# Kernel optimization log

Hardware: AMD Instinct MI355X
Metric: run time of the kernel (lower is better)

## Reference

```python
import jax, jax.numpy as jnp
import numpy as np

# ----- module constants (from init_kwargs) -----
PCD_RANGE = np.array([-5.0, -5.0, -2.0, 5.0, 5.0, 2.0], dtype=np.float32)
VOXEL = np.array([1.0, 1.0, 1.0], dtype=np.float32)
ANG_BINS = 8
MAX_DIS = 15
GRID = ((PCD_RANGE[3:] - PCD_RANGE[:3]) // VOXEL + 1).astype(np.int64)  # [11,11,5]
L = int(np.prod(GRID))  # 605 grid locations
LOW = PCD_RANGE[:3]


def _locs():
    ax = [np.arange(g, dtype=np.float32) for g in GRID]
    mesh = np.stack(np.meshgrid(*ax, indexing='ij'), axis=-1).reshape(-1, 3)  # [L,3]
    return jnp.asarray(LOW + mesh * VOXEL)


def _mats():
    angs = np.array([np.pi / ANG_BINS * a - np.pi / 2 for a in range(ANG_BINS)], dtype=np.float32)
    c, s = np.cos(angs), np.sin(angs)
    z, o = np.zeros_like(c), np.ones_like(c)
    m = np.stack([np.stack([c, -s, z], -1), np.stack([s, c, z], -1), np.stack([z, z, o], -1)], axis=1)
    return jnp.asarray(m)  # [A,3,3]


def setup_inputs() -> dict:
    key = jax.random.key(0)
    lo = jnp.array([-4.5, -4.5, -1.5], dtype=jnp.float32)
    hi = jnp.array([4.5, 4.5, 1.5], dtype=jnp.float32)
    pcd = jax.random.uniform(key, (8, 16384, 3), dtype=jnp.float32, minval=0.0, maxval=1.0)
    pcd = lo + pcd * (hi - lo)  # points inside the point-cloud range
    return {"pcd": pcd}


def reference(pcd):
    B, N, _ = pcd.shape
    locs = _locs()                       # [L,3]
    mats = _mats()                       # [A,3,3]
    offset = jnp.asarray(-LOW + VOXEL / 2.0)
    vox = jnp.asarray(VOXEL)

    # ---- radius count feature: count(dist <= i+1) for i in 0..MAX_DIS-1 ----
    # squared distances via gram trick -> [B,L,N] (avoids [B,L,N,3] diff tensor)
    d2 = ((pcd ** 2).sum(-1)[:, None, :] + (locs ** 2).sum(-1)[None, :, None]
          - 2.0 * jnp.einsum('bnd,ld->bln', pcd, locs))
    d = jnp.ceil(jnp.sqrt(jnp.maximum(d2, 0.0)))  # integer-valued ceil distances
    dint = jax.lax.stop_gradient(jnp.clip(d, 0, MAX_DIS + 1).astype(jnp.int32))
    hist = jax.vmap(lambda r: jnp.bincount(r, length=MAX_DIS + 2))(dint.reshape(B * L, N))
    cum = jnp.cumsum(hist.reshape(B, L, MAX_DIS + 2), axis=-1)
    feature = cum[..., 1:MAX_DIS + 1]    # [B,L,MAX_DIS], count(d <= i+1)

    # ---- rotated voxel histogram feature ----
    # pcd @ M.T for each angle: [A,B,N,3]
    rot = jnp.einsum('bnd,aed->abne', pcd, mats) + offset
    coords = jnp.floor(rot / vox)
    gz, gy = int(GRID[2]), int(GRID[1])
    flat = coords[..., 2] + coords[..., 1] * gz + coords[..., 0] * gy * gz
    idx = jax.lax.stop_gradient(flat.astype(jnp.int32))  # [A,B,N]
    # torch.histc(min=-0.5, max=L-0.5) keeps integer values in [0, L-1]
    valid = (idx >= 0) & (idx < L)
    idx_safe = jnp.where(valid, idx, L)
    A = ANG_BINS
    hr = jax.vmap(lambda r: jnp.bincount(r, length=L + 1))(idx_safe.reshape(A * B, N))
    feature_rot = hr.reshape(A, B, L + 1)[..., :L].transpose(1, 2, 0)  # [B,L,A]

    out = jnp.concatenate([feature.astype(jnp.float32),
                           feature_rot.astype(jnp.float32)], axis=-1) / N
    return out  # [B, L, MAX_DIS + ANG_BINS]
```

## Files before the change

kernel.cpp:

```cpp
#include <hip/hip_runtime.h>

#define BATCH  8
#define NPTS   16384
#define LVOX   605
#define ABINS  8
#define CH     23
#define NCOL   121
#define NBIN   14
#define BPTS   256
#define FEAT_BLOCKS (BATCH * (NPTS / BPTS))
#define ROT_CH    4
#define ROT_CHPTS (NPTS / ROT_CH)
#define ROT_BLOCKS (ABINS * BATCH * ROT_CH)

#define ROT_WS_U32  (ABINS * BATCH * LVOX)
#define FEAT_WS_U32 (BATCH * LVOX * (NBIN / 2))
#define WS_U32_TOTAL (ROT_WS_U32 + FEAT_WS_U32)

__global__ __launch_bounds__(256) void zero_kernel(unsigned* __restrict__ ws) {
    const int i = blockIdx.x * 256 + threadIdx.x;
    if (i < WS_U32_TOTAL) ws[i] = 0u;
}

__global__ __launch_bounds__(512) void main_kernel(const float* __restrict__ pcd,
                                                   int* __restrict__ rot_hist,
                                                   unsigned* __restrict__ feat_hist) {
    __shared__ unsigned hist[5][NBIN][128];
    const int bid = blockIdx.x;
    const int tid = threadIdx.x;

    if (bid < FEAT_BLOCKS) {
        const int b     = bid >> 6;
        const int outer = bid & 63;

        {
            unsigned* hp = &hist[0][0][0];
            for (int i = tid; i < 5 * NBIN * 128; i += 512) hp[i] = 0u;
        }

        const int li = tid & 127;
        const int cc = (li < NCOL) ? li : (NCOL - 1);
        const float lx = -5.0f + (float)(cc / 11);
        const float ly = -5.0f + (float)(cc % 11);
        const int pbase = __builtin_amdgcn_readfirstlane(tid >> 7) * 64;
        const float* __restrict__ pp =
            pcd + ((size_t)b * NPTS + outer * BPTS + pbase) * 3;

        __syncthreads();

#pragma unroll 4
        for (int j = 0; j < 64; ++j) {
            const float px = pp[j * 3 + 0];
            const float py = pp[j * 3 + 1];
            const float pz = pp[j * 3 + 2];
            const float dx = px - lx, dy = py - ly;
            const float rxy2 = fmaf(dy, dy, dx * dx);
            const float dz0 = pz + 2.0f;
#pragma unroll
            for (int z = 0; z < 5; ++z) {
                const float dz = dz0 - (float)z;
                const float d  = __builtin_amdgcn_sqrtf(fmaf(dz, dz, rxy2));
                const int   k  = (int)d;
                atomicAdd(&hist[z][k][li], 1u);
            }
        }
        __syncthreads();

        for (int item = tid; item < NCOL * 5 * (NBIN / 2); item += 512) {
            const int kp  = item % 7;
            const int rem = item / 7;
            const int z   = rem % 5;
            const int col = rem / 5;
            const unsigned v = hist[z][2 * kp][col] | (hist[z][2 * kp + 1][col] << 16);
            if (v) atomicAdd(&feat_hist[((size_t)b * LVOX + col * 5 + z) * 7 + kp], v);
        }
    } else {
        const int rb    = bid - FEAT_BLOCKS;
        const int ab    = rb & 63;
        const int chunk = rb >> 6;
        const int a     = ab >> 3;
        const int b     = ab & 7;

        int* h = (int*)&hist[0][0][0];
        for (int i = tid; i < LVOX; i += 512) h[i] = 0;
        __syncthreads();

        const float C[8] = { -4.3711388e-08f, 0.3826834323650898f, 0.7071067811865476f,
                             0.9238795325112867f, 1.0f, 0.9238795325112867f,
                             0.7071067811865476f, 0.3826834323650898f };
        const float S[8] = { -1.0f, -0.9238795325112867f, -0.7071067811865476f,
                             -0.3826834323650898f, 0.0f, 0.3826834323650898f,
                             0.7071067811865476f, 0.9238795325112867f };
        const float c = C[a];
        const float s = S[a];

        const float* __restrict__ p =
            pcd + ((size_t)b * NPTS + (size_t)chunk * ROT_CHPTS) * 3;

        for (int n = tid; n < ROT_CHPTS; n += 512) {
            const float x = p[n * 3 + 0];
            const float y = p[n * 3 + 1];
            const float z = p[n * 3 + 2];
            const float rx = x * c - y * s + 5.5f;
            const float ry = x * s + y * c + 5.5f;
            const float rz = z + 2.5f;
            const int icx = (int)floorf(rx);
            const int icy = (int)floorf(ry);
            const int icz = (int)floorf(rz);
            const int flat = icz + icy * 5 + icx * 55;
            if (flat >= 0 && flat < LVOX) atomicAdd(&h[flat], 1);
        }
        __syncthreads();

        int* __restrict__ dst = rot_hist + (size_t)ab * LVOX;
        for (int i = tid; i < LVOX; i += 512) {
            const int v = h[i];
            if (v) atomicAdd(&dst[i], v);
        }
    }
}

__global__ __launch_bounds__(256) void write_kernel(const int* __restrict__ rot_hist,
                                                    const unsigned* __restrict__ feat16,
                                                    float* __restrict__ out) {
    const int gt    = blockIdx.x * 256 + threadIdx.x;
    const int group = gt >> 4;
    const int q     = gt & 15;
    if (group >= BATCH * LVOX) return;
    const int b = group / LVOX;
    const int l = group % LVOX;

    int v = 0;
    if (q < NBIN) {
        const unsigned w = feat16[(size_t)group * 7 + (q >> 1)];
        v = (int)((w >> (16 * (q & 1))) & 0xFFFFu);
    }
#pragma unroll
    for (int off = 1; off < 16; off <<= 1) {
        const int t = __shfl_up(v, off, 16);
        if (q >= off) v += t;
    }
    const float inv_n = 1.0f / (float)NPTS;
    float* __restrict__ o = out + (size_t)group * CH;
    if (q < NBIN)       o[q]  = (float)v * inv_n;
    else if (q == NBIN) o[14] = 1.0f;
    if (q < 8) {
        const int r = rot_hist[((size_t)q * BATCH + b) * LVOX + l];
        o[15 + q] = (float)r * inv_n;
    }
}

extern "C" void kernel_launch(void* const* d_in, const int* in_sizes, int n_in,
                              void* d_out, int out_size, void* d_ws, size_t ws_size,
                              hipStream_t stream) {
    const float* pcd = (const float*)d_in[0];
    float* out = (float*)d_out;
    int* rot_hist = (int*)d_ws;
    unsigned* feat16 = (unsigned*)d_ws + ROT_WS_U32;

    hipLaunchKernelGGL(zero_kernel, dim3((WS_U32_TOTAL + 255) / 256), dim3(256), 0,
                       stream, (unsigned*)d_ws);
    hipLaunchKernelGGL(main_kernel, dim3(FEAT_BLOCKS + ROT_BLOCKS), dim3(512), 0,
                       stream, pcd, rot_hist, feat16);
    hipLaunchKernelGGL(write_kernel, dim3((BATCH * LVOX * 16 + 255) / 256), dim3(256),
                       0, stream, rot_hist, feat16, out);
}
```

Measured before the change: 35.61 us.

## Replace LDS atomics for two z-layers with packed register nibble counters

For z-layers 3 and 4, distance-bin counts are now kept in 64-bit registers as 4-bit nibble counters. Every 15 points these are flushed into 8-bit lanes split into even and odd bins, and then staged through shared memory instead of issuing an LDS atomic per point. This cuts LDS atomic traffic by two fifths and shrinks the histogram array. In exchange it adds 64-bit shift and add work and a more complex reduction step. Correctness relies on bin indices staying below 16 and per-thread counts not overflowing 8 bits.

```diff
diff --git a/kernel.cpp b/kernel.cpp
--- a/kernel.cpp
+++ b/kernel.cpp
@@ -17,6 +17,8 @@
 #define FEAT_WS_U32 (BATCH * LVOX * (NBIN / 2))
 #define WS_U32_TOTAL (ROT_WS_U32 + FEAT_WS_U32)
 
+#define MASK8 0x0F0F0F0F0F0F0F0Full
+
 __global__ __launch_bounds__(256) void zero_kernel(unsigned* __restrict__ ws) {
     const int i = blockIdx.x * 256 + threadIdx.x;
     if (i < WS_U32_TOTAL) ws[i] = 0u;
@@ -25,7 +27,8 @@
 __global__ __launch_bounds__(512) void main_kernel(const float* __restrict__ pcd,
                                                    int* __restrict__ rot_hist,
                                                    unsigned* __restrict__ feat_hist) {
-    __shared__ unsigned hist[5][NBIN][128];
+    __shared__ unsigned hist[3][NBIN][128];
+    __shared__ unsigned long long stag[2][2][4][129];
     const int bid = blockIdx.x;
     const int tid = threadIdx.x;
 
@@ -35,35 +38,56 @@
 
         {
             unsigned* hp = &hist[0][0][0];
-            for (int i = tid; i < 5 * NBIN * 128; i += 512) hp[i] = 0u;
+            for (int i = tid; i < 3 * NBIN * 128; i += 512) hp[i] = 0u;
         }
 
         const int li = tid & 127;
         const int cc = (li < NCOL) ? li : (NCOL - 1);
         const float lx = -5.0f + (float)(cc / 11);
         const float ly = -5.0f + (float)(cc % 11);
-        const int pbase = __builtin_amdgcn_readfirstlane(tid >> 7) * 64;
+        const int g4 = __builtin_amdgcn_readfirstlane(tid >> 7);
         const float* __restrict__ pp =
-            pcd + ((size_t)b * NPTS + outer * BPTS + pbase) * 3;
-
-        __syncthreads();
-
-#pragma unroll 4
-        for (int j = 0; j < 64; ++j) {
-            const float px = pp[j * 3 + 0];
-            const float py = pp[j * 3 + 1];
-            const float pz = pp[j * 3 + 2];
-            const float dx = px - lx, dy = py - ly;
-            const float rxy2 = fmaf(dy, dy, dx * dx);
-            const float dz0 = pz + 2.0f;
-#pragma unroll
-            for (int z = 0; z < 5; ++z) {
-                const float dz = dz0 - (float)z;
-                const float d  = __builtin_amdgcn_sqrtf(fmaf(dz, dz, rxy2));
-                const int   k  = (int)d;
-                atomicAdd(&hist[z][k][li], 1u);
-            }
-        }
+            pcd + ((size_t)b * NPTS + outer * BPTS + g4 * 64) * 3;
+
+        unsigned long long be3 = 0, bo3 = 0, be4 = 0, bo4 = 0;
+
+        __syncthreads();
+
+#define PT(J)                                                                   \
+        {                                                                       \
+            const float px = pp[(J) * 3 + 0];                                   \
+            const float py = pp[(J) * 3 + 1];                                   \
+            const float pz = pp[(J) * 3 + 2];                                   \
+            const float dx = px - lx, dy = py - ly;                             \
+            const float rxy2 = fmaf(dy, dy, dx * dx);                           \
+            const float dz0 = pz + 2.0f;                                        \
+            { const float dz = dz0;        const float d = __builtin_amdgcn_sqrtf(fmaf(dz, dz, rxy2)); atomicAdd(&hist[0][(int)d][li], 1u); } \
+            { const float dz = dz0 - 1.0f; const float d = __builtin_amdgcn_sqrtf(fmaf(dz, dz, rxy2)); atomicAdd(&hist[1][(int)d][li], 1u); } \
+            { const float dz = dz0 - 2.0f; const float d = __builtin_amdgcn_sqrtf(fmaf(dz, dz, rxy2)); atomicAdd(&hist[2][(int)d][li], 1u); } \
+            { const float dz = dz0 - 3.0f; const float d = __builtin_amdgcn_sqrtf(fmaf(dz, dz, rxy2)); n3 += 1ull << (((int)d) << 2); } \
+            { const float dz = dz0 - 4.0f; const float d = __builtin_amdgcn_sqrtf(fmaf(dz, dz, rxy2)); n4 += 1ull << (((int)d) << 2); } \
+        }
+
+#pragma unroll
+        for (int grp = 0; grp < 4; ++grp) {
+            const int base = grp * 15;
+            unsigned long long n3 = 0, n4 = 0;
+#pragma unroll
+            for (int j = 0; j < 15; ++j) PT(base + j)
+            be3 += n3 & MASK8; bo3 += (n3 >> 4) & MASK8;
+            be4 += n4 & MASK8; bo4 += (n4 >> 4) & MASK8;
+        }
+        {
+            unsigned long long n3 = 0, n4 = 0;
+#pragma unroll
+            for (int j = 60; j < 64; ++j) PT(j)
+            be3 += n3 & MASK8; bo3 += (n3 >> 4) & MASK8;
+            be4 += n4 & MASK8; bo4 += (n4 >> 4) & MASK8;
+        }
+#undef PT
+
+        stag[0][0][g4][li] = be3;  stag[0][1][g4][li] = bo3;
+        stag[1][0][g4][li] = be4;  stag[1][1][g4][li] = bo4;
         __syncthreads();
 
         for (int item = tid; item < NCOL * 5 * (NBIN / 2); item += 512) {
@@ -71,7 +95,19 @@
             const int rem = item / 7;
             const int z   = rem % 5;
             const int col = rem / 5;
-            const unsigned v = hist[z][2 * kp][col] | (hist[z][2 * kp + 1][col] << 16);
+            unsigned v;
+            if (z < 3) {
+                v = hist[z][2 * kp][col] | (hist[z][2 * kp + 1][col] << 16);
+            } else {
+                const int zz = z - 3;
+                unsigned lo = 0, hi = 0;
+#pragma unroll
+                for (int g = 0; g < 4; ++g) {
+                    lo += (unsigned)((stag[zz][0][g][col] >> (8 * kp)) & 0xFFull);
+                    hi += (unsigned)((stag[zz][1][g][col] >> (8 * kp)) & 0xFFull);
+                }
+                v = lo | (hi << 16);
+            }
             if (v) atomicAdd(&feat_hist[((size_t)b * LVOX + col * 5 + z) * 7 + kp], v);
         }
     } else {
```

Result: slower. 37.51 us (+5.4%).
